# Performance work log

Measured on AMD Instinct MI355X. Metric: run time of the kernel, lower is better.

## Reference

```python
import jax, jax.numpy as jnp
import numpy as np

INPLANES = 768
HIDDEN = 64
NUM_EXPERTS = 6
TOP_K = 2


def setup_inputs() -> dict:
    key = jax.random.key(0)
    ks = jax.random.split(key, 7)
    B, C, D = 64, 320, INPLANES
    x = jax.random.normal(ks[0], (B, C, D), dtype=jnp.float32)
    xi = jax.random.normal(ks[1], (B, C, D), dtype=jnp.float32)
    # gating network: per-token logits over experts
    w_gate = jax.random.normal(ks[2], (D, NUM_EXPERTS), dtype=jnp.float32) / np.sqrt(D)
    # LoRA-style experts: down-projection D -> HIDDEN per expert
    expert_w = jax.random.normal(ks[3], (NUM_EXPERTS, D, HIDDEN), dtype=jnp.float32) / np.sqrt(D)
    expert_b = jnp.zeros((NUM_EXPERTS, HIDDEN), dtype=jnp.float32)
    # reprojection ffn1_1: Linear(HIDDEN, INPLANES), torch convention W:[out,in]
    ffn1_w = jax.random.normal(ks[4], (D, HIDDEN), dtype=jnp.float32) / np.sqrt(HIDDEN)
    ffn1_b = jnp.zeros((D,), dtype=jnp.float32)
    return {"x": x, "xi": xi, "w_gate": w_gate, "expert_w": expert_w,
            "expert_b": expert_b, "ffn1_w": ffn1_w, "ffn1_b": ffn1_b}


def _cv_squared(v):
    eps = 1e-10
    return jnp.var(v) / (jnp.mean(v) ** 2 + eps)


def reference(x, xi, w_gate, expert_w, expert_b, ffn1_w, ffn1_b):
    B, C, D = x.shape
    nz = C // 5
    # slice template (z) and search (x) token streams from both modalities
    z0, x0 = x[:, :nz, :], x[:, nz:, :]
    z1, x1 = xi[:, :nz, :], xi[:, nz:, :]
    # MoE_lora: fuse the two modalities and route tokens (z tokens first, then x)
    inp = jnp.concatenate([z0 + z1, x0 + x1], axis=1)        # [B, C, D]
    tok = inp.reshape(-1, D)                                  # [N, D], N = B*C
    N = tok.shape[0]
    # noisy-top-k gating (clean/eval path): top-2 experts, softmax over kept logits
    logits = tok @ w_gate                                     # [N, E]
    top_vals, top_idx = jax.lax.top_k(logits, TOP_K)          # [N, k]
    top_gates = jax.nn.softmax(top_vals, axis=-1)             # [N, k]
    gates = jnp.zeros_like(logits).at[jnp.arange(N)[:, None], top_idx].add(top_gates)
    # expert LoRA down-projections, combined by sparse gates (dense-equivalent math)
    h = jnp.einsum('nd,edh->enh', tok, expert_w) + expert_b[:, None, :]  # [E, N, H]
    y = jnp.einsum('ne,enh->nh', gates, h)                    # [N, H]
    y = y.reshape(B, C, HIDDEN)
    z_moe, x_moe = y[:, :nz, :], y[:, nz:, :]
    # load-balancing loss: cv^2 of importance + cv^2 of load
    importance = gates.sum(axis=0)
    load = (gates > 0).astype(jnp.float32).sum(axis=0)
    loss = _cv_squared(importance) + _cv_squared(load)
    # ffn1_1 reprojection back to inplanes
    x_prompted = x_moe @ ffn1_w.T + ffn1_b                    # [B, 4C/5, D]
    z_prompted = z_moe @ ffn1_w.T + ffn1_b                    # [B, C/5, D]
    return (x_prompted, z_prompted, loss, logits)
```

## Files before the change

kernel.cpp:

```cpp
#include <hip/hip_runtime.h>

typedef __attribute__((ext_vector_type(8))) short short8;
typedef __attribute__((ext_vector_type(4))) short short4v;
typedef __attribute__((ext_vector_type(4))) float f32x4;

#define VM(n) asm volatile("s_waitcnt vmcnt(" #n ")" ::: "memory")
#define LGKM0 asm volatile("s_waitcnt lgkmcnt(0)" ::: "memory")

namespace {

constexpr int DIN  = 768;
constexpr int HID  = 64;
constexpr int NEXP = 6;
constexpr int CDIM  = 320;
constexpr int NZ    = 64;
constexpr int NTOK  = 20480;

constexpr long long XP_OFF   = 0;
constexpr long long ZP_OFF   = 12582912LL;
constexpr long long LOSS_OFF = 15728640LL;
constexpr long long LG_OFF   = 15728641LL;

__device__ inline unsigned short f2bf(float f) {
  union { float f; unsigned u; } v{f};
  return (unsigned short)((v.u + 0x7FFFu + ((v.u >> 16) & 1u)) >> 16);
}
__device__ inline float b2f(unsigned short s) {
  union { unsigned u; float f; } v{(unsigned)s << 16};
  return v.f;
}
__device__ inline void gload16(const void* g, void* l) {
  __builtin_amdgcn_global_load_lds(
      (const __attribute__((address_space(1))) unsigned*)g,
      (__attribute__((address_space(3))) unsigned*)l, 16, 0, 0);
}
__device__ inline int row_base(int n) {
  int bb = n / CDIM, c = n - bb * CDIM;
  return (c < NZ) ? (int)(ZP_OFF + (long long)(bb * NZ + c) * DIN)
                  : (int)(XP_OFF + (long long)(bb * (CDIM - NZ) + (c - NZ)) * DIN);
}

__global__ __launch_bounds__(256) void pre_kernel(
    const float* __restrict__ x, const float* __restrict__ xi,
    const float* __restrict__ wg, const float* __restrict__ ew,
    const float* __restrict__ fw,
    float* __restrict__ out, float4* __restrict__ rec,
    unsigned short* __restrict__ ewb_t, unsigned short* __restrict__ fwb)
{
  int b = blockIdx.x, tid = threadIdx.x;
  __shared__ __align__(16) char sbuf[21504];
  if (b < 72) {
    float (*t_lds)[65] = (float(*)[65])sbuf;
    int e = b / 12, kc = (b % 12) * 64;
    const float* src = ew + (size_t)e * DIN * HID + (size_t)kc * HID;
    #pragma unroll
    for (int it = 0; it < 16; ++it) {
      int f = it * 256 + tid; int ky = f >> 6, h = f & 63;
      t_lds[h][ky] = src[ky * 64 + h];
    }
    __syncthreads();
    unsigned short* dst = ewb_t + (size_t)e * DIN * HID + kc;
    #pragma unroll
    for (int it = 0; it < 16; ++it) {
      int f = it * 256 + tid; int h = f >> 6, ky = f & 63;
      dst[(size_t)h * DIN + ky] = f2bf(t_lds[h][ky]);
    }
    return;
  }
  if (b < 84) {
    int base = (b - 72) * 4096;
    #pragma unroll
    for (int it = 0; it < 16; ++it) {
      int idx = base + it * 256 + tid;
      fwb[idx] = f2bf(fw[idx]);
    }
    return;
  }
  float* wgl = (float*)sbuf;
  for (int i = tid; i < NEXP * DIN; i += 256) {
    int d = i / 6, e = i - d * 6;
    wgl[(d >> 2) * 28 + (d & 3) * 6 + e] = wg[i];
  }
  __syncthreads();

  int lane = tid & 63, wid = tid >> 6;
  int ls = lane & 15;
  int n  = (b - 84) * 16 + wid * 4 + (lane >> 4);

  const float4* xv  = reinterpret_cast<const float4*>(x  + (size_t)n * DIN);
  const float4* iv  = reinterpret_cast<const float4*>(xi + (size_t)n * DIN);
  unsigned short* tk = (unsigned short*)out + (size_t)row_base(n) * 2;

  float lg[NEXP];
  #pragma unroll
  for (int e = 0; e < NEXP; ++e) lg[e] = 0.f;

  #pragma unroll
  for (int k = 0; k < 12; ++k) {
    float4 a = xv[ls + 16 * k];
    float4 q = iv[ls + 16 * k];
    float tv0 = a.x + q.x, tv1 = a.y + q.y, tv2 = a.z + q.z, tv3 = a.w + q.w;
    short4v t4;
    t4[0] = (short)f2bf(tv0); t4[1] = (short)f2bf(tv1);
    t4[2] = (short)f2bf(tv2); t4[3] = (short)f2bf(tv3);
    *(short4v*)(tk + ls * 4 + 64 * k) = t4;
    const float4* wq = (const float4*)(wgl + (ls + 16 * k) * 28);
    float4 w0 = wq[0], w1 = wq[1], w2 = wq[2], w3 = wq[3], w4 = wq[4], w5 = wq[5];
    lg[0] += tv0 * w0.x; lg[1] += tv0 * w0.y; lg[2] += tv0 * w0.z;
    lg[3] += tv0 * w0.w; lg[4] += tv0 * w1.x; lg[5] += tv0 * w1.y;
    lg[0] += tv1 * w1.z; lg[1] += tv1 * w1.w; lg[2] += tv1 * w2.x;
    lg[3] += tv1 * w2.y; lg[4] += tv1 * w2.z; lg[5] += tv1 * w2.w;
    lg[0] += tv2 * w3.x; lg[1] += tv2 * w3.y; lg[2] += tv2 * w3.z;
    lg[3] += tv2 * w3.w; lg[4] += tv2 * w4.x; lg[5] += tv2 * w4.y;
    lg[0] += tv3 * w4.z; lg[1] += tv3 * w4.w; lg[2] += tv3 * w5.x;
    lg[3] += tv3 * w5.y; lg[4] += tv3 * w5.z; lg[5] += tv3 * w5.w;
  }
  #pragma unroll
  for (int e = 0; e < NEXP; ++e) {
    float v = lg[e];
    v += __shfl_xor(v, 1, 64);
    v += __shfl_xor(v, 2, 64);
    v += __shfl_xor(v, 4, 64);
    v += __shfl_xor(v, 8, 64);
    lg[e] = v;
  }
  int e0 = 0; float v0 = lg[0];
  #pragma unroll
  for (int j = 1; j < NEXP; ++j) if (lg[j] > v0) { v0 = lg[j]; e0 = j; }
  int e1 = 0; float v1 = -3.4e38f;
  #pragma unroll
  for (int j = 0; j < NEXP; ++j) if (j != e0 && lg[j] > v1) { v1 = lg[j]; e1 = j; }
  float g0 = 1.f / (1.f + expf(v1 - v0));
  if (ls < NEXP) {
    float myv = lg[0];
    #pragma unroll
    for (int e = 1; e < NEXP; ++e) if (ls == e) myv = lg[e];
    out[LG_OFF + (size_t)n * NEXP + ls] = myv;
  }
  if (ls == 0) rec[n] = make_float4((float)e0, (float)e1, g0, 1.f - g0);
}

__global__ __launch_bounds__(512) void moe_kernel(
    const unsigned short* __restrict__ ewb_t, const float* __restrict__ eb,
    const unsigned short* __restrict__ fwb, const float* __restrict__ fb,
    const float4* __restrict__ rec, float* __restrict__ out)
{
  __shared__ __align__(16) char smem[74752];
  __shared__ int rb[64];
  __shared__ float simp[8][NEXP], sld[8][NEXP];

  int tid = threadIdx.x, lane = tid & 63, wid = tid >> 6;
  int qw = lane >> 4, l15 = lane & 15;
  int wm = wid >> 2, wn = wid & 3;

  if (blockIdx.x == 320) {
    float imp[NEXP], ld[NEXP];
    #pragma unroll
    for (int e = 0; e < NEXP; ++e) { imp[e] = 0.f; ld[e] = 0.f; }
    for (int n = tid; n < NTOK; n += 512) {
      float4 r = rec[n];
      int e0 = (int)r.x, e1 = (int)r.y;
      #pragma unroll
      for (int e = 0; e < NEXP; ++e) {
        imp[e] += (e == e0 ? r.z : 0.f) + (e == e1 ? r.w : 0.f);
        ld[e]  += (e == e0 ? 1.f : 0.f) + (e == e1 ? 1.f : 0.f);
      }
    }
    #pragma unroll
    for (int e = 0; e < NEXP; ++e) {
      float a = imp[e], bq = ld[e];
      #pragma unroll
      for (int off = 32; off >= 1; off >>= 1) {
        a += __shfl_xor(a, off, 64);
        bq += __shfl_xor(bq, off, 64);
      }
      imp[e] = a; ld[e] = bq;
    }
    if (lane == 0) {
      #pragma unroll
      for (int e = 0; e < NEXP; ++e) { simp[wid][e] = imp[e]; sld[wid][e] = ld[e]; }
    }
    __syncthreads();
    if (tid == 0) {
      float It[NEXP], Lt[NEXP], mi = 0.f, ml = 0.f;
      #pragma unroll
      for (int e = 0; e < NEXP; ++e) {
        It[e] = 0.f; Lt[e] = 0.f;
        #pragma unroll
        for (int w = 0; w < 8; ++w) { It[e] += simp[w][e]; Lt[e] += sld[w][e]; }
        mi += It[e]; ml += Lt[e];
      }
      mi /= NEXP; ml /= NEXP;
      float vi = 0.f, vl = 0.f;
      #pragma unroll
      for (int e = 0; e < NEXP; ++e) {
        vi += (It[e] - mi) * (It[e] - mi);
        vl += (Lt[e] - ml) * (Lt[e] - ml);
      }
      vi /= NEXP; vl /= NEXP;
      out[LOSS_OFF] = vi / (mi * mi + 1e-10f) + vl / (ml * ml + 1e-10f);
    }
    return;
  }

  int t0 = blockIdx.x * 64;
  const unsigned short* tokb = (const unsigned short*)out;

  size_t b_src[3]; int b_dst[3];
  #pragma unroll
  for (int it = 0; it < 3; ++it) {
    int F = it * 512 + tid, r = F >> 2, s = F & 3;
    b_src[it] = (size_t)r * DIN + ((s ^ (r & 3) ^ ((r & 4) >> 1)) << 3);
    b_dst[it] = (it * 512 + wid * 64) * 16;
  }
  int ar = tid >> 2, as = tid & 3;
  size_t a_src = (size_t)row_base(t0 + ar) * 2 +
                 ((as ^ (ar & 3) ^ ((ar & 4) >> 1)) << 3);
  int a_dst = (wid * 64) * 16;

  if (tid < 64) rb[tid] = row_base(t0 + tid);

  #pragma unroll
  for (int it = 0; it < 3; ++it)
    gload16(ewb_t + b_src[it], smem + 8192 + b_dst[it]);
  if (tid < 256) gload16(tokb + a_src, smem + a_dst);

  f32x4 acc[2][6];
  #pragma unroll
  for (int m = 0; m < 2; ++m)
    #pragma unroll
    for (int n = 0; n < 6; ++n) acc[m][n] = (f32x4){0.f, 0.f, 0.f, 0.f};

  int aoff[2], boff[6];
  #pragma unroll
  for (int m = 0; m < 2; ++m) {
    int row = wm * 32 + m * 16 + l15;
    aoff[m] = row * 64 + ((qw ^ (row & 3) ^ ((row & 4) >> 1)) << 4);
  }
  #pragma unroll
  for (int n = 0; n < 6; ++n) {
    int row = wn * 96 + n * 16 + l15;
    boff[n] = row * 64 + ((qw ^ (row & 3) ^ ((row & 4) >> 1)) << 4);
  }

  for (int k = 0; k < 24; ++k) {
    const char* cA = smem + (k & 1) * 4096;
    const char* cB = smem + 8192 + (k & 1) * 24576;
    char* nA = (char*)smem + ((k + 1) & 1) * 4096;
    char* nB = (char*)smem + 8192 + ((k + 1) & 1) * 24576;
    if (k < 23) {
      #pragma unroll
      for (int it = 0; it < 3; ++it)
        gload16(ewb_t + b_src[it] + (k + 1) * 32, nB + b_dst[it]);
      if (tid < 256) gload16(tokb + a_src + (k + 1) * 32, nA + a_dst);
      if (wid < 4) VM(4); else VM(3);
    } else {
      VM(0);
    }
    __builtin_amdgcn_s_barrier();
    __builtin_amdgcn_sched_barrier(0);
    short8 af[2], bfv[6];
    #pragma unroll
    for (int m = 0; m < 2; ++m) af[m] = *(const short8*)(cA + aoff[m]);
    #pragma unroll
    for (int n = 0; n < 6; ++n) bfv[n] = *(const short8*)(cB + boff[n]);
    __builtin_amdgcn_s_setprio(1);
    #pragma unroll
    for (int m = 0; m < 2; ++m)
      #pragma unroll
      for (int n = 0; n < 6; ++n)
        acc[m][n] = __builtin_amdgcn_mfma_f32_16x16x32_bf16(af[m], bfv[n], acc[m][n], 0, 0, 0);
    __builtin_amdgcn_s_setprio(0);
    __builtin_amdgcn_sched_barrier(0);
    __builtin_amdgcn_s_barrier();
  }

  #pragma unroll
  for (int it = 0; it < 2; ++it) {
    int F = it * 512 + tid, r = F >> 3, s = F & 7;
    gload16(fwb + (size_t)r * HID + ((s ^ (r & 7)) << 3),
            smem + 58368 + (it * 512 + wid * 64) * 16);
  }

  unsigned short* hl = (unsigned short*)(smem + 8192);
  #pragma unroll
  for (int m = 0; m < 2; ++m)
    #pragma unroll
    for (int n = 0; n < 6; ++n)
      #pragma unroll
      for (int i = 0; i < 4; ++i) {
        int row = wm * 32 + m * 16 + qw * 4 + i;
        int col = wn * 96 + n * 16 + l15;
        hl[row * 392 + col] = f2bf(acc[m][n][i]);
      }
  LGKM0;
  __builtin_amdgcn_s_barrier();

  {
    int t = tid >> 3, j0 = (tid & 7) * 8;
    float4 rr = rec[t0 + t];
    int e0 = (int)rr.x, e1 = (int)rr.y;
    float g0 = rr.z, g1 = rr.w;
    short8 h0 = *(const short8*)(hl + t * 392 + e0 * 64 + j0);
    short8 h1 = *(const short8*)(hl + t * 392 + e1 * 64 + j0);
    const float4* ep0 = (const float4*)(eb + e0 * 64 + j0);
    const float4* ep1 = (const float4*)(eb + e1 * 64 + j0);
    float4 b0a = ep0[0], b0b = ep0[1], b1a = ep1[0], b1b = ep1[1];
    float be0[8] = {b0a.x, b0a.y, b0a.z, b0a.w, b0b.x, b0b.y, b0b.z, b0b.w};
    float be1[8] = {b1a.x, b1a.y, b1a.z, b1a.w, b1b.x, b1b.y, b1b.z, b1b.w};
    short8 ov;
    #pragma unroll
    for (int j = 0; j < 8; ++j) {
      float v = g0 * (b2f((unsigned short)h0[j]) + be0[j])
              + g1 * (b2f((unsigned short)h1[j]) + be1[j]);
      ov[j] = (short)f2bf(v);
    }
    *(short8*)(smem + t * 128 + ((((tid & 7)) ^ (t & 7)) << 4)) = ov;
  }
  LGKM0;
  __builtin_amdgcn_s_barrier();

  for (int c = 0; c < 6; ++c) {
    const char* cF = smem + ((c & 1) ? 8192 : 58368);
    char* nF = (char*)smem + ((c & 1) ? 58368 : 8192);
    if (c < 5) {
      #pragma unroll
      for (int it = 0; it < 2; ++it) {
        int F = it * 512 + tid, r = F >> 3, s = F & 7;
        gload16(fwb + (size_t)((c + 1) * 128 + r) * HID + ((s ^ (r & 7)) << 3),
                nF + (it * 512 + wid * 64) * 16);
      }
      VM(2);
    } else {
      VM(0);
    }
    __builtin_amdgcn_s_barrier();
    __builtin_amdgcn_sched_barrier(0);
    f32x4 a2[2][2];
    #pragma unroll
    for (int m = 0; m < 2; ++m)
      #pragma unroll
      for (int n = 0; n < 2; ++n) a2[m][n] = (f32x4){0.f, 0.f, 0.f, 0.f};
    #pragma unroll
    for (int kk = 0; kk < 2; ++kk) {
      short8 ay[2], bw[2];
      #pragma unroll
      for (int m = 0; m < 2; ++m) {
        int row = wm * 32 + m * 16 + l15;
        ay[m] = *(const short8*)(smem + row * 128 + (((kk * 4 + qw) ^ (row & 7)) << 4));
      }
      #pragma unroll
      for (int n = 0; n < 2; ++n) {
        int rw = wn * 32 + n * 16 + l15;
        bw[n] = *(const short8*)(cF + rw * 128 + (((kk * 4 + qw) ^ (rw & 7)) << 4));
      }
      __builtin_amdgcn_s_setprio(1);
      #pragma unroll
      for (int m = 0; m < 2; ++m)
        #pragma unroll
        for (int n = 0; n < 2; ++n)
          a2[m][n] = __builtin_amdgcn_mfma_f32_16x16x32_bf16(ay[m], bw[n], a2[m][n], 0, 0, 0);
      __builtin_amdgcn_s_setprio(0);
    }
    #pragma unroll
    for (int n = 0; n < 2; ++n) {
      int col = c * 128 + wn * 32 + n * 16 + l15;
      float bias = fb[col];
      #pragma unroll
      for (int m = 0; m < 2; ++m)
        #pragma unroll
        for (int i = 0; i < 4; ++i) {
          int rl = wm * 32 + m * 16 + qw * 4 + i;
          out[(size_t)rb[rl] + col] = a2[m][n][i] + bias;
        }
    }
    __builtin_amdgcn_sched_barrier(0);
    __builtin_amdgcn_s_barrier();
  }
}

}

extern "C" void kernel_launch(void* const* d_in, const int* in_sizes, int n_in,
                              void* d_out, int out_size, void* d_ws, size_t ws_size,
                              hipStream_t stream)
{
  const float* x  = (const float*)d_in[0];
  const float* xi = (const float*)d_in[1];
  const float* wg = (const float*)d_in[2];
  const float* ew = (const float*)d_in[3];
  const float* eb = (const float*)d_in[4];
  const float* fw = (const float*)d_in[5];
  const float* fb = (const float*)d_in[6];
  float* out = (float*)d_out;

  char* w = (char*)d_ws;
  float4*         rec   = (float4*)w;
  unsigned short* ewb_t = (unsigned short*)(w + 327680);
  unsigned short* fwb   = (unsigned short*)(w + 327680 + 589824);

  pre_kernel<<<84 + 1280, 256, 0, stream>>>(x, xi, wg, ew, fw, out, rec, ewb_t, fwb);
  moe_kernel<<<321, 512, 0, stream>>>(ewb_t, eb, fwb, fb, rec, out);
}
```

Before: 67.41 us.

## Double-buffer x/xi token loads through LDS with async global_load_lds in pre_kernel

The gating/token-sum phase of pre_kernel now streams x and xi rows into a double-buffered LDS region using async global-to-LDS loads, prefetching chunk k+1 while chunk k is processed. The aim is to overlap global memory latency with the logit FMAs instead of relying on direct float4 register loads. The cost is more LDS per block (lower occupancy possible), two barriers per iteration, and a loop that is no longer unrolled. Each lane's read offset maps back to the bytes it loaded itself, so the data layout works out.

New measurement: 70.05 us. 3.9% more time.

```diff
diff --git a/kernel.cpp b/kernel.cpp
--- a/kernel.cpp
+++ b/kernel.cpp
@@ -48,7 +48,7 @@
     unsigned short* __restrict__ ewb_t, unsigned short* __restrict__ fwb)
 {
   int b = blockIdx.x, tid = threadIdx.x;
-  __shared__ __align__(16) char sbuf[21504];
+  __shared__ __align__(16) char sbuf[37888];
   if (b < 72) {
     float (*t_lds)[65] = (float(*)[65])sbuf;
     int e = b / 12, kc = (b % 12) * 64;
@@ -81,24 +81,42 @@
     int d = i / 6, e = i - d * 6;
     wgl[(d >> 2) * 28 + (d & 3) * 6 + e] = wg[i];
   }
-  __syncthreads();
-
-  int lane = tid & 63, wid = tid >> 6;
-  int ls = lane & 15;
-  int n  = (b - 84) * 16 + wid * 4 + (lane >> 4);
-
-  const float4* xv  = reinterpret_cast<const float4*>(x  + (size_t)n * DIN);
-  const float4* iv  = reinterpret_cast<const float4*>(xi + (size_t)n * DIN);
+
+  int ls = tid & 15;
+  int ti = tid >> 4;
+  int t0 = (b - 84) * 16;
+  int n  = t0 + ti;
+  int wid = tid >> 6;
+
+  const float* xsrc = x  + (size_t)n * DIN + ls * 4;
+  const float* isrc = xi + (size_t)n * DIN + ls * 4;
+  char* bufb = sbuf + 21504;
+  int soff = wid * 1024 + (tid & 63) * 16;
+
   unsigned short* tk = (unsigned short*)out + (size_t)row_base(n) * 2;
 
   float lg[NEXP];
   #pragma unroll
   for (int e = 0; e < NEXP; ++e) lg[e] = 0.f;
 
-  #pragma unroll
+  gload16(xsrc, bufb + soff);
+  gload16(isrc, bufb + 4096 + soff);
+  LGKM0;
+
   for (int k = 0; k < 12; ++k) {
-    float4 a = xv[ls + 16 * k];
-    float4 q = iv[ls + 16 * k];
+    char* cur = bufb + (k & 1) * 8192;
+    char* nxt = bufb + ((k + 1) & 1) * 8192;
+    if (k < 11) {
+      gload16(xsrc + (k + 1) * 64, nxt + soff);
+      gload16(isrc + (k + 1) * 64, nxt + 4096 + soff);
+      VM(2);
+    } else {
+      VM(0);
+    }
+    __builtin_amdgcn_s_barrier();
+    __builtin_amdgcn_sched_barrier(0);
+    float4 a = *(const float4*)(cur + ti * 256 + ls * 16);
+    float4 q = *(const float4*)(cur + 4096 + ti * 256 + ls * 16);
     float tv0 = a.x + q.x, tv1 = a.y + q.y, tv2 = a.z + q.z, tv3 = a.w + q.w;
     short4v t4;
     t4[0] = (short)f2bf(tv0); t4[1] = (short)f2bf(tv1);
@@ -114,7 +132,10 @@
     lg[3] += tv2 * w3.w; lg[4] += tv2 * w4.x; lg[5] += tv2 * w4.y;
     lg[0] += tv3 * w4.z; lg[1] += tv3 * w4.w; lg[2] += tv3 * w5.x;
     lg[3] += tv3 * w5.y; lg[4] += tv3 * w5.z; lg[5] += tv3 * w5.w;
-  }
+    LGKM0;
+    __builtin_amdgcn_s_barrier();
+  }
+
   #pragma unroll
   for (int e = 0; e < NEXP; ++e) {
     float v = lg[e];
```
